# Kernel optimization log

Hardware: AMD Instinct MI355X
Metric: run time of the kernel (lower is better)

Reference implementation:

```python
import jax, jax.numpy as jnp
import numpy as np

B, H, S, D = 4, 16, 2048, 64
SCALE = float(D ** 0.5)


def setup_inputs() -> dict:
    key = jax.random.key(0)
    kq, kk, kv = jax.random.split(key, 3)
    q = jax.random.normal(kq, (B, H, S, D), dtype=jnp.float32)
    k = jax.random.normal(kk, (B, H, S, D), dtype=jnp.float32)
    v = jax.random.normal(kv, (B, H, S, D), dtype=jnp.float32)
    return {"q": q, "k": k, "v": v}


def reference(q, k, v):
    # score: (B, H, S, S)
    score = jnp.einsum('bhqd,bhkd->bhqk', q, k) / SCALE
    seq_len = q.shape[-2]
    # causal mask: True above the diagonal (future positions) -> -inf
    mask = jnp.triu(jnp.ones((seq_len, seq_len), dtype=bool), k=1)
    score = jnp.where(mask, -jnp.inf, score)
    attn = jax.nn.softmax(score, axis=-1)
    return jnp.einsum('bhqk,bhkd->bhqd', attn, v)
```

## Files before the change

### kernel.cpp

```cpp
#include <hip/hip_runtime.h>
#include <math.h>

constexpr int S = 2048, D = 64;
constexpr int BH = 64;
constexpr int QTILE = 256;
constexpr int KVB = 64;
constexpr int NQT = S / QTILE;
constexpr float QSCALE = 0.18033688011112042f;
constexpr float DMTHR = 5.0f;

typedef float f32x4 __attribute__((ext_vector_type(4)));
typedef float f32x16 __attribute__((ext_vector_type(16)));
typedef _Float16 f16x8 __attribute__((ext_vector_type(8)));
typedef _Float16 f16x4 __attribute__((ext_vector_type(4)));
typedef unsigned int u32;
typedef unsigned int u32x4 __attribute__((ext_vector_type(4)));

#define MFMA32(a, b, c) __builtin_amdgcn_mfma_f32_32x32x16_f16((a), (b), (c), 0, 0, 0)

#if __has_builtin(__builtin_amdgcn_exp2f)
#define EXP2(x) __builtin_amdgcn_exp2f(x)
#else
#define EXP2(x) exp2f(x)
#endif

#define MAX3(a, b, c) fmaxf(fmaxf((a), (b)), (c))

__device__ __forceinline__ u32 pkbits(float a, float b) {
  return __builtin_bit_cast(u32, __builtin_amdgcn_cvt_pkrtz(a, b));
}
__device__ __forceinline__ void plswap(u32& a, u32& b) {
  asm volatile("v_permlane32_swap_b32 %0, %1" : "+v"(a), "+v"(b));
}
__device__ __forceinline__ int swzb(int row) { return ((row & 7) ^ (row >> 3)) << 3; }

__device__ __forceinline__ void compute_tile(
    const int kt, const int Rp, const int q32, const int hi,
    const _Float16* __restrict__ Kb, const _Float16* __restrict__ Vb,
    const f16x8 (&bq)[4], f32x16& od0, f32x16& od1, float& m, float& l) {
  const int ck = kt * KVB;
  if (ck > Rp + 31) return;
  const int rel = Rp - ck;
  const int ctmax = (rel >= 32) ? 1 : 0;
  const bool needmask = (32 * ctmax + 31 > rel);

  f32x16 st0 = {}, st1 = {};
  __builtin_amdgcn_s_setprio(1);
#pragma unroll
  for (int t = 0; t < 4; ++t) {
    f16x8 a = *(const f16x8*)&Kb[(q32 << 6) + (swzb(q32) ^ (16 * t + 8 * hi))];
    st0 = MFMA32(a, bq[t], st0);
  }
  if (ctmax) {
    const int row = 32 + q32;
#pragma unroll
    for (int t = 0; t < 4; ++t) {
      f16x8 a = *(const f16x8*)&Kb[(row << 6) + (swzb(row) ^ (16 * t + 8 * hi))];
      st1 = MFMA32(a, bq[t], st1);
    }
  }
  __builtin_amdgcn_s_setprio(0);

  if (needmask) {
    const int qrel = rel + q32;
#pragma unroll
    for (int gq = 0; gq < 4; ++gq)
#pragma unroll
      for (int i = 0; i < 4; ++i) {
        if (8 * gq + 4 * hi + i > qrel) st0[4 * gq + i] = -INFINITY;
        if (ctmax && (32 + 8 * gq + 4 * hi + i > qrel)) st1[4 * gq + i] = -INFINITY;
      }
  }

  float pmax;
  {
    const float a0 = MAX3(st0[0], st0[1], st0[2]);
    const float a1 = MAX3(st0[3], st0[4], st0[5]);
    const float a2 = MAX3(st0[6], st0[7], st0[8]);
    const float a3 = MAX3(st0[9], st0[10], st0[11]);
    const float a4 = MAX3(st0[12], st0[13], st0[14]);
    const float b0 = MAX3(a0, a1, st0[15]);
    const float b1 = fmaxf(a2, a3);
    pmax = MAX3(b0, b1, a4);
  }
  if (ctmax) {
    const float a0 = MAX3(st1[0], st1[1], st1[2]);
    const float a1 = MAX3(st1[3], st1[4], st1[5]);
    const float a2 = MAX3(st1[6], st1[7], st1[8]);
    const float a3 = MAX3(st1[9], st1[10], st1[11]);
    const float a4 = MAX3(st1[12], st1[13], st1[14]);
    const float b0 = MAX3(a0, a1, st1[15]);
    const float b1 = MAX3(a2, a3, pmax);
    pmax = MAX3(b0, b1, a4);
  }
  pmax = fmaxf(pmax, __shfl_xor(pmax, 32));

  if (!__all(pmax - m <= DMTHR)) {
    const float mn = fmaxf(m, pmax);
    const float alpha = EXP2(m - mn);
    m = mn;
    l *= alpha;
#pragma unroll
    for (int r = 0; r < 16; ++r) od0[r] *= alpha;
#pragma unroll
    for (int r = 0; r < 16; ++r) od1[r] *= alpha;
  }

  float ps = 0.f;
#pragma unroll
  for (int r = 0; r < 16; ++r) { const float p = EXP2(st0[r] - m); st0[r] = p; ps += p; }
  if (ctmax)
#pragma unroll
    for (int r = 0; r < 16; ++r) { const float p = EXP2(st1[r] - m); st1[r] = p; ps += p; }
  l += ps;

  __builtin_amdgcn_s_setprio(1);
#define PV_CT(stv, CT)                                                          \
  _Pragma("unroll")                                                             \
  for (int t = 0; t < 2; ++t) {                                                 \
    u32 x0 = pkbits(stv[8 * t + 0], stv[8 * t + 1]);                            \
    u32 x1 = pkbits(stv[8 * t + 2], stv[8 * t + 3]);                            \
    u32 y0 = pkbits(stv[8 * t + 4], stv[8 * t + 5]);                            \
    u32 y1 = pkbits(stv[8 * t + 6], stv[8 * t + 7]);                            \
    plswap(x0, y0); plswap(x1, y1);                                             \
    const f16x8 pf = __builtin_bit_cast(f16x8, (u32x4){x0, x1, y0, y1});        \
    const int kcol = (2 * (CT) + t) * 16 + 8 * hi;                              \
    { const f16x8 vf = *(const f16x8*)&Vb[(q32 << 6) + (swzb(q32) ^ kcol)];     \
      od0 = MFMA32(vf, pf, od0); }                                              \
    { const int row = 32 + q32;                                                 \
      const f16x8 vf = *(const f16x8*)&Vb[(row << 6) + (swzb(row) ^ kcol)];     \
      od1 = MFMA32(vf, pf, od1); }                                              \
  }
  PV_CT(st0, 0);
  if (ctmax) { PV_CT(st1, 1); }
#undef PV_CT
  __builtin_amdgcn_s_setprio(0);
}

__global__ __launch_bounds__(512, 2)
void attn_fwd(const float* __restrict__ qp, const float* __restrict__ kp,
              const float* __restrict__ vp, float* __restrict__ op) {
  __shared__ _Float16 Kl[4][KVB * 64];
  __shared__ _Float16 Vt[4][64 * KVB];

  const int bh = blockIdx.x;
  constexpr int g8[8] = {7, 6, 5, 4, 0, 1, 2, 3};
  const int qt = g8[blockIdx.y];

  const int tid = threadIdx.x;
  const int wid = tid >> 6;
  const int lane = tid & 63;
  const int q32 = lane & 31;
  const int hi = lane >> 5;

  const size_t base = (size_t)bh * (S * D);
  const int Rp = qt * QTILE + wid * 32;

  f16x8 bq[4];
  {
    const float* qg = qp + base + (size_t)(Rp + q32) * D + 8 * hi;
#pragma unroll
    for (int t = 0; t < 4; ++t) {
      f32x4 a = *(const f32x4*)(qg + 16 * t);
      f32x4 b = *(const f32x4*)(qg + 16 * t + 4);
#pragma unroll
      for (int j = 0; j < 4; ++j) bq[t][j] = (_Float16)(a[j] * QSCALE);
#pragma unroll
      for (int j = 0; j < 4; ++j) bq[t][4 + j] = (_Float16)(b[j] * QSCALE);
    }
  }

  f32x16 od0 = {}, od1 = {};
  float m = -INFINITY, l = 0.f;

  const int NT = 4 * qt + 4;

  const int rp = tid >> 4;
  const int cg = tid & 15;
  const int r0 = 2 * rp, r1 = 2 * rp + 1;
  const int c4 = cg * 4;
  const int kw0 = (r0 << 6) + (swzb(r0) ^ c4);
  const int kw1 = (r1 << 6) + (swzb(r1) ^ c4);
  const int vw0 = ((c4 + 0) << 6) + (swzb(c4 + 0) ^ r0);
  const int vw1 = ((c4 + 1) << 6) + (swzb(c4 + 1) ^ r0);
  const int vw2 = ((c4 + 2) << 6) + (swzb(c4 + 2) ^ r0);
  const int vw3 = ((c4 + 3) << 6) + (swzb(c4 + 3) ^ r0);

#define LOADT(kt, K0, K1, V0, V1)                                        \
  do {                                                                   \
    const float* kg_ = kp + base + (size_t)((kt) * KVB + r0) * D + c4;   \
    const float* vg_ = vp + base + (size_t)((kt) * KVB + r0) * D + c4;   \
    K0 = *(const f32x4*)kg_; K1 = *(const f32x4*)(kg_ + D);              \
    V0 = *(const f32x4*)vg_; V1 = *(const f32x4*)(vg_ + D);              \
  } while (0)

#define WRITET(buf, K0, K1, V0, V1)                                      \
  do {                                                                   \
    f16x4 k0h_, k1h_;                                                    \
    _Pragma("unroll")                                                    \
    for (int j = 0; j < 4; ++j) {                                        \
      k0h_[j] = (_Float16)K0[j]; k1h_[j] = (_Float16)K1[j];              \
    }                                                                    \
    *(f16x4*)&Kl[buf][kw0] = k0h_;                                       \
    *(f16x4*)&Kl[buf][kw1] = k1h_;                                       \
    *(u32*)&Vt[buf][vw0] = pkbits(V0[0], V1[0]);                         \
    *(u32*)&Vt[buf][vw1] = pkbits(V0[1], V1[1]);                         \
    *(u32*)&Vt[buf][vw2] = pkbits(V0[2], V1[2]);                         \
    *(u32*)&Vt[buf][vw3] = pkbits(V0[3], V1[3]);                         \
  } while (0)

  f32x4 ka0, ka1, va0, va1, kb0, kb1, vb0, vb1;
  LOADT(0, ka0, ka1, va0, va1);
  LOADT(1, kb0, kb1, vb0, vb1);

  for (int ktp = 0; ktp < NT; ktp += 2) {
    const int b0 = ktp & 2;
    WRITET(b0, ka0, ka1, va0, va1);
    WRITET(b0 + 1, kb0, kb1, vb0, vb1);
    if (ktp + 2 < NT) LOADT(ktp + 2, ka0, ka1, va0, va1);
    __syncthreads();
    compute_tile(ktp, Rp, q32, hi, Kl[b0], Vt[b0], bq, od0, od1, m, l);
    if (ktp + 3 < NT) LOADT(ktp + 3, kb0, kb1, vb0, vb1);
    compute_tile(ktp + 1, Rp, q32, hi, Kl[b0 + 1], Vt[b0 + 1], bq, od0, od1, m, l);
  }
#undef LOADT
#undef WRITET

  const float lt = l + __shfl_xor(l, 32);
  const float inv = 1.f / lt;
  float* og = op + base + (size_t)(Rp + q32) * D + 4 * hi;
#pragma unroll
  for (int gq = 0; gq < 4; ++gq) {
    f32x4 w0, w1;
#pragma unroll
    for (int i = 0; i < 4; ++i) w0[i] = od0[4 * gq + i] * inv;
#pragma unroll
    for (int i = 0; i < 4; ++i) w1[i] = od1[4 * gq + i] * inv;
    *(f32x4*)(og + 8 * gq) = w0;
    *(f32x4*)(og + 32 + 8 * gq) = w1;
  }
}

extern "C" void kernel_launch(void* const* d_in, const int* in_sizes, int n_in,
                              void* d_out, int out_size, void* d_ws, size_t ws_size,
                              hipStream_t stream) {
  const float* q = (const float*)d_in[0];
  const float* k = (const float*)d_in[1];
  const float* v = (const float*)d_in[2];
  float* out = (float*)d_out;
  dim3 grid(BH, NQT);
  attn_fwd<<<grid, 512, 0, stream>>>(q, k, v, out);
}
```

Baseline: 69.83 us.

## Halve query tile to 128 rows with 4 warps and single-tile double buffering

```diff
diff --git a/kernel.cpp b/kernel.cpp
--- a/kernel.cpp
+++ b/kernel.cpp
@@ -3,7 +3,7 @@
 
 constexpr int S = 2048, D = 64;
 constexpr int BH = 64;
-constexpr int QTILE = 256;
+constexpr int QTILE = 128;
 constexpr int KVB = 64;
 constexpr int NQT = S / QTILE;
 constexpr float QSCALE = 0.18033688011112042f;
@@ -137,15 +137,15 @@
   __builtin_amdgcn_s_setprio(0);
 }
 
-__global__ __launch_bounds__(512, 2)
+__global__ __launch_bounds__(256, 3)
 void attn_fwd(const float* __restrict__ qp, const float* __restrict__ kp,
               const float* __restrict__ vp, float* __restrict__ op) {
-  __shared__ _Float16 Kl[4][KVB * 64];
-  __shared__ _Float16 Vt[4][64 * KVB];
+  __shared__ _Float16 Kl[2][KVB * 64];
+  __shared__ _Float16 Vt[2][64 * KVB];
 
   const int bh = blockIdx.x;
-  constexpr int g8[8] = {7, 6, 5, 4, 0, 1, 2, 3};
-  const int qt = g8[blockIdx.y];
+  constexpr int g16[16] = {15, 1, 11, 5, 0, 14, 4, 10, 13, 3, 9, 7, 2, 12, 6, 8};
+  const int qt = g16[blockIdx.y];
 
   const int tid = threadIdx.x;
   const int wid = tid >> 6;
@@ -173,55 +173,60 @@
   f32x16 od0 = {}, od1 = {};
   float m = -INFINITY, l = 0.f;
 
-  const int NT = 4 * qt + 4;
-
-  const int rp = tid >> 4;
+  const int NT = 2 * qt + 2;
+
+  const int pr = tid >> 4;
   const int cg = tid & 15;
-  const int r0 = 2 * rp, r1 = 2 * rp + 1;
+  const int rA = 2 * pr, rB = 2 * pr + 32;
   const int c4 = cg * 4;
-  const int kw0 = (r0 << 6) + (swzb(r0) ^ c4);
-  const int kw1 = (r1 << 6) + (swzb(r1) ^ c4);
-  const int vw0 = ((c4 + 0) << 6) + (swzb(c4 + 0) ^ r0);
-  const int vw1 = ((c4 + 1) << 6) + (swzb(c4 + 1) ^ r0);
-  const int vw2 = ((c4 + 2) << 6) + (swzb(c4 + 2) ^ r0);
-  const int vw3 = ((c4 + 3) << 6) + (swzb(c4 + 3) ^ r0);
-
-#define LOADT(kt, K0, K1, V0, V1)                                        \
+  const int kwA0 = ((rA + 0) << 6) + (swzb(rA + 0) ^ c4);
+  const int kwA1 = ((rA + 1) << 6) + (swzb(rA + 1) ^ c4);
+  const int kwB0 = ((rB + 0) << 6) + (swzb(rB + 0) ^ c4);
+  const int kwB1 = ((rB + 1) << 6) + (swzb(rB + 1) ^ c4);
+  int vwA[4], vwB[4];
+#pragma unroll
+  for (int j = 0; j < 4; ++j) {
+    const int d = c4 + j;
+    vwA[j] = (d << 6) + (swzb(d) ^ rA);
+    vwB[j] = (d << 6) + (swzb(d) ^ rB);
+  }
+
+#define LOADT(kt)                                                        \
   do {                                                                   \
-    const float* kg_ = kp + base + (size_t)((kt) * KVB + r0) * D + c4;   \
-    const float* vg_ = vp + base + (size_t)((kt) * KVB + r0) * D + c4;   \
-    K0 = *(const f32x4*)kg_; K1 = *(const f32x4*)(kg_ + D);              \
-    V0 = *(const f32x4*)vg_; V1 = *(const f32x4*)(vg_ + D);              \
+    const float* kg_ = kp + base + (size_t)((kt) * KVB + rA) * D + c4;   \
+    const float* vg_ = vp + base + (size_t)((kt) * KVB + rA) * D + c4;   \
+    ka0 = *(const f32x4*)kg_;            ka1 = *(const f32x4*)(kg_ + D); \
+    kb0 = *(const f32x4*)(kg_ + 32 * D); kb1 = *(const f32x4*)(kg_ + 33 * D); \
+    va0 = *(const f32x4*)vg_;            va1 = *(const f32x4*)(vg_ + D); \
+    vb0 = *(const f32x4*)(vg_ + 32 * D); vb1 = *(const f32x4*)(vg_ + 33 * D); \
   } while (0)
 
-#define WRITET(buf, K0, K1, V0, V1)                                      \
+#define WRITET(buf)                                                      \
   do {                                                                   \
-    f16x4 k0h_, k1h_;                                                    \
+    f16x4 h0, h1, h2, h3;                                                \
     _Pragma("unroll")                                                    \
     for (int j = 0; j < 4; ++j) {                                        \
-      k0h_[j] = (_Float16)K0[j]; k1h_[j] = (_Float16)K1[j];              \
+      h0[j] = (_Float16)ka0[j]; h1[j] = (_Float16)ka1[j];                \
+      h2[j] = (_Float16)kb0[j]; h3[j] = (_Float16)kb1[j];                \
     }                                                                    \
-    *(f16x4*)&Kl[buf][kw0] = k0h_;                                       \
-    *(f16x4*)&Kl[buf][kw1] = k1h_;                                       \
-    *(u32*)&Vt[buf][vw0] = pkbits(V0[0], V1[0]);                         \
-    *(u32*)&Vt[buf][vw1] = pkbits(V0[1], V1[1]);                         \
-    *(u32*)&Vt[buf][vw2] = pkbits(V0[2], V1[2]);                         \
-    *(u32*)&Vt[buf][vw3] = pkbits(V0[3], V1[3]);                         \
+    *(f16x4*)&Kl[buf][kwA0] = h0;  *(f16x4*)&Kl[buf][kwA1] = h1;         \
+    *(f16x4*)&Kl[buf][kwB0] = h2;  *(f16x4*)&Kl[buf][kwB1] = h3;         \
+    _Pragma("unroll")                                                    \
+    for (int j = 0; j < 4; ++j) {                                        \
+      *(u32*)&Vt[buf][vwA[j]] = pkbits(va0[j], va1[j]);                  \
+      *(u32*)&Vt[buf][vwB[j]] = pkbits(vb0[j], vb1[j]);                  \
+    }                                                                    \
   } while (0)
 
-  f32x4 ka0, ka1, va0, va1, kb0, kb1, vb0, vb1;
-  LOADT(0, ka0, ka1, va0, va1);
-  LOADT(1, kb0, kb1, vb0, vb1);
-
-  for (int ktp = 0; ktp < NT; ktp += 2) {
-    const int b0 = ktp & 2;
-    WRITET(b0, ka0, ka1, va0, va1);
-    WRITET(b0 + 1, kb0, kb1, vb0, vb1);
-    if (ktp + 2 < NT) LOADT(ktp + 2, ka0, ka1, va0, va1);
+  f32x4 ka0, ka1, kb0, kb1, va0, va1, vb0, vb1;
+  LOADT(0);
+
+  for (int kt = 0; kt < NT; ++kt) {
+    const int buf = kt & 1;
+    WRITET(buf);
+    if (kt + 1 < NT) LOADT(kt + 1);
     __syncthreads();
-    compute_tile(ktp, Rp, q32, hi, Kl[b0], Vt[b0], bq, od0, od1, m, l);
-    if (ktp + 3 < NT) LOADT(ktp + 3, kb0, kb1, vb0, vb1);
-    compute_tile(ktp + 1, Rp, q32, hi, Kl[b0 + 1], Vt[b0 + 1], bq, od0, od1, m, l);
+    compute_tile(kt, Rp, q32, hi, Kl[buf], Vt[buf], bq, od0, od1, m, l);
   }
 #undef LOADT
 #undef WRITET
@@ -249,5 +254,5 @@
   const float* v = (const float*)d_in[2];
   float* out = (float*)d_out;
   dim3 grid(BH, NQT);
-  attn_fwd<<<grid, 512, 0, stream>>>(q, k, v, out);
-}
+  attn_fwd<<<grid, 256, 0, stream>>>(q, k, v, out);
+}
```

After: 75.45 us. +8.1%, slower.
